# Performance work log

Hardware: AMD Instinct MI355X
Metric: run time of the kernel (lower is better)

The kernel has to match this reference:

```python
import jax, jax.numpy as jnp
import numpy as np

CD_COEFF = 1.0


def setup_inputs() -> dict:
    key = jax.random.key(0)
    k1, k2 = jax.random.split(key)
    x_diff_pred = jax.random.normal(k1, (16, 2048, 3), dtype=jnp.float32)
    x_diff_target = jax.random.normal(k2, (16, 2048, 3), dtype=jnp.float32)
    return {"x_diff_pred": x_diff_pred, "x_diff_target": x_diff_target}


def _chamfer(p1, p2):
    # p1: (bs, N, 3), p2: (bs, M, 3)
    # squared pairwise distances: (bs, N, M)
    diff = p1[:, :, None, :] - p2[:, None, :, :]
    d2 = jnp.sum(diff * diff, axis=-1)
    # bidirectional min reduction
    min_p1 = jnp.min(d2, axis=2)  # (bs, N): nearest target for each pred point
    min_p2 = jnp.min(d2, axis=1)  # (bs, M): nearest pred for each target point
    return jnp.mean(min_p1) + jnp.mean(min_p2)


def reference(x_diff_pred, x_diff_target):
    cd = _chamfer(x_diff_pred, x_diff_target)
    return CD_COEFF * cd
```

## Files before the change

kernel.cpp:

```cpp
#include <hip/hip_runtime.h>


#define NPTS  2048
#define BATCH 16
#define NBLK  256

__global__ __launch_bounds__(1024) void chamfer_kernel(
    const float* __restrict__ pred,
    const float* __restrict__ tgt,
    float* __restrict__ partial)
{
    const int bid = blockIdx.x;
    const int dir = bid >> 7;
    const int b   = (bid >> 3) & 15;
    const int qc  = bid & 7;

    const int tid  = threadIdx.x;
    const int lane = tid & 63;
    const int w    = tid >> 6;

    const float* __restrict__ P = dir ? tgt  : pred;
    const float* __restrict__ T = dir ? pred : tgt;
    const float* Pb = P + (size_t)b * NPTS * 3;
    const float* Tb = T + (size_t)b * NPTS * 3;

    __shared__ float4 tile[NPTS];
    __shared__ float  smin[16][256];
    __shared__ float  spart[4];

    #pragma unroll
    for (int k = 0; k < 2; ++k) {
        const int idx = tid + k * 1024;
        const float x = Tb[idx * 3 + 0];
        const float y = Tb[idx * 3 + 1];
        const float z = Tb[idx * 3 + 2];
        tile[idx] = make_float4(x, y, z, x * x + y * y + z * z);
    }

    float qx[4], qy[4], qz[4], pp[4], m0[4], m1[4];
    #pragma unroll
    for (int q = 0; q < 4; ++q) {
        const int qi = qc * 256 + q * 64 + lane;
        const float x = Pb[qi * 3 + 0];
        const float y = Pb[qi * 3 + 1];
        const float z = Pb[qi * 3 + 2];
        qx[q] = -2.0f * x;
        qy[q] = -2.0f * y;
        qz[q] = -2.0f * z;
        pp[q] = x * x + y * y + z * z;
        m0[q] = 3.4e38f;
        m1[q] = 3.4e38f;
    }

    __syncthreads();

    const int base = w * 128;
    #pragma unroll 2
    for (int j = 0; j < 128; j += 4) {
        const float4 ta = tile[base + j + 0];
        const float4 tb = tile[base + j + 1];
        const float4 tc = tile[base + j + 2];
        const float4 td = tile[base + j + 3];
        #pragma unroll
        for (int q = 0; q < 4; ++q) {
            const float da = fmaf(qz[q], ta.z, fmaf(qy[q], ta.y, fmaf(qx[q], ta.x, ta.w)));
            const float db = fmaf(qz[q], tb.z, fmaf(qy[q], tb.y, fmaf(qx[q], tb.x, tb.w)));
            const float dc = fmaf(qz[q], tc.z, fmaf(qy[q], tc.y, fmaf(qx[q], tc.x, tc.w)));
            const float dd = fmaf(qz[q], td.z, fmaf(qy[q], td.y, fmaf(qx[q], td.x, td.w)));
            m0[q] = fminf(fminf(m0[q], da), db);
            m1[q] = fminf(fminf(m1[q], dc), dd);
        }
    }

    #pragma unroll
    for (int q = 0; q < 4; ++q)
        smin[w][q * 64 + lane] = fminf(m0[q], m1[q]) + pp[q];
    __syncthreads();

    if (tid < 256) {
        float v = smin[0][tid];
        #pragma unroll
        for (int ww = 1; ww < 16; ++ww)
            v = fminf(v, smin[ww][tid]);
        #pragma unroll
        for (int off = 32; off > 0; off >>= 1)
            v += __shfl_down(v, off);
        if (lane == 0)
            spart[w] = v;
    }
    __syncthreads();

    if (tid == 0)
        partial[bid] = spart[0] + spart[1] + spart[2] + spart[3];
}

__global__ __launch_bounds__(256) void reduce_kernel(
    const float* __restrict__ partial,
    float* __restrict__ out)
{
    const int tid  = threadIdx.x;
    const int lane = tid & 63;
    const int w    = tid >> 6;
    __shared__ float s[4];

    float v = partial[tid];
    #pragma unroll
    for (int off = 32; off > 0; off >>= 1)
        v += __shfl_down(v, off);
    if (lane == 0) s[w] = v;
    __syncthreads();

    if (tid == 0)
        out[0] = (s[0] + s[1] + s[2] + s[3]) * (1.0f / (float)(BATCH * NPTS));
}

extern "C" void kernel_launch(void* const* d_in, const int* in_sizes, int n_in,
                              void* d_out, int out_size, void* d_ws, size_t ws_size,
                              hipStream_t stream)
{
    const float* pred = (const float*)d_in[0];
    const float* tgt  = (const float*)d_in[1];
    float* out = (float*)d_out;
    float* partial = (float*)d_ws;

    chamfer_kernel<<<dim3(NBLK), dim3(1024), 0, stream>>>(pred, tgt, partial);
    reduce_kernel<<<dim3(1), dim3(256), 0, stream>>>(partial, out);
}
```

Baseline: 17.72 us.

## Fuse final reduction into main kernel via last-block atomic counter; prefetch LDS tiles

Result: slower. 27.87 us (+57.3%).

```diff
diff --git a/kernel.cpp b/kernel.cpp
--- a/kernel.cpp
+++ b/kernel.cpp
@@ -8,7 +8,9 @@
 __global__ __launch_bounds__(1024) void chamfer_kernel(
     const float* __restrict__ pred,
     const float* __restrict__ tgt,
-    float* __restrict__ partial)
+    float* __restrict__ partial,
+    unsigned int* __restrict__ counter,
+    float* __restrict__ out)
 {
     const int bid = blockIdx.x;
     const int dir = bid >> 7;
@@ -27,6 +29,7 @@
     __shared__ float4 tile[NPTS];
     __shared__ float  smin[16][256];
     __shared__ float  spart[4];
+    __shared__ int    slast;
 
     #pragma unroll
     for (int k = 0; k < 2; ++k) {
@@ -55,12 +58,18 @@
     __syncthreads();
 
     const int base = w * 128;
+    float4 ta = tile[base + 0];
+    float4 tb = tile[base + 1];
+    float4 tc = tile[base + 2];
+    float4 td = tile[base + 3];
+
     #pragma unroll 2
     for (int j = 0; j < 128; j += 4) {
-        const float4 ta = tile[base + j + 0];
-        const float4 tb = tile[base + j + 1];
-        const float4 tc = tile[base + j + 2];
-        const float4 td = tile[base + j + 3];
+        const int nj = base + ((j + 4) & 127);
+        const float4 na = tile[nj + 0];
+        const float4 nb = tile[nj + 1];
+        const float4 nc = tile[nj + 2];
+        const float4 nd = tile[nj + 3];
         #pragma unroll
         for (int q = 0; q < 4; ++q) {
             const float da = fmaf(qz[q], ta.z, fmaf(qy[q], ta.y, fmaf(qx[q], ta.x, ta.w)));
@@ -70,6 +79,7 @@
             m0[q] = fminf(fminf(m0[q], da), db);
             m1[q] = fminf(fminf(m1[q], dc), dd);
         }
+        ta = na; tb = nb; tc = nc; td = nd;
     }
 
     #pragma unroll
@@ -90,28 +100,31 @@
     }
     __syncthreads();
 
-    if (tid == 0)
-        partial[bid] = spart[0] + spart[1] + spart[2] + spart[3];
-}
-
-__global__ __launch_bounds__(256) void reduce_kernel(
-    const float* __restrict__ partial,
-    float* __restrict__ out)
-{
-    const int tid  = threadIdx.x;
-    const int lane = tid & 63;
-    const int w    = tid >> 6;
-    __shared__ float s[4];
-
-    float v = partial[tid];
-    #pragma unroll
-    for (int off = 32; off > 0; off >>= 1)
-        v += __shfl_down(v, off);
-    if (lane == 0) s[w] = v;
+    if (tid == 0) {
+        const float s = spart[0] + spart[1] + spart[2] + spart[3];
+        __hip_atomic_store(&partial[bid], s, __ATOMIC_RELEASE,
+                           __HIP_MEMORY_SCOPE_AGENT);
+        const unsigned int old = __hip_atomic_fetch_add(
+            counter, 1u, __ATOMIC_ACQ_REL, __HIP_MEMORY_SCOPE_AGENT);
+        slast = (old == NBLK - 1);
+    }
     __syncthreads();
 
-    if (tid == 0)
-        out[0] = (s[0] + s[1] + s[2] + s[3]) * (1.0f / (float)(BATCH * NPTS));
+    if (slast) {
+        if (tid < 256) {
+            float v = __hip_atomic_load(&partial[tid], __ATOMIC_RELAXED,
+                                        __HIP_MEMORY_SCOPE_AGENT);
+            #pragma unroll
+            for (int off = 32; off > 0; off >>= 1)
+                v += __shfl_down(v, off);
+            if (lane == 0)
+                spart[w] = v;
+        }
+        __syncthreads();
+        if (tid == 0)
+            out[0] = (spart[0] + spart[1] + spart[2] + spart[3])
+                     * (1.0f / (float)(BATCH * NPTS));
+    }
 }
 
 extern "C" void kernel_launch(void* const* d_in, const int* in_sizes, int n_in,
@@ -122,7 +135,10 @@
     const float* tgt  = (const float*)d_in[1];
     float* out = (float*)d_out;
     float* partial = (float*)d_ws;
+    unsigned int* counter = (unsigned int*)((char*)d_ws + NBLK * sizeof(float));
 
-    chamfer_kernel<<<dim3(NBLK), dim3(1024), 0, stream>>>(pred, tgt, partial);
-    reduce_kernel<<<dim3(1), dim3(256), 0, stream>>>(partial, out);
+    hipMemsetAsync(counter, 0, sizeof(unsigned int), stream);
+
+    chamfer_kernel<<<dim3(NBLK), dim3(1024), 0, stream>>>(pred, tgt, partial,
+                                                          counter, out);
 }
```

## Split target set across block pairs and give each thread eight queries

Applied to the files above, without the earlier changes.

Result: slower. 22.58 us (+27.4%).

```diff
diff --git a/kernel.cpp b/kernel.cpp
--- a/kernel.cpp
+++ b/kernel.cpp
@@ -4,6 +4,8 @@
 #define NPTS  2048
 #define BATCH 16
 #define NBLK  256
+#define QPB   512
+#define TPB   1024
 
 __global__ __launch_bounds__(1024) void chamfer_kernel(
     const float* __restrict__ pred,
@@ -13,7 +15,8 @@
     const int bid = blockIdx.x;
     const int dir = bid >> 7;
     const int b   = (bid >> 3) & 15;
-    const int qc  = bid & 7;
+    const int qc  = (bid >> 1) & 3;
+    const int th  = bid & 1;
 
     const int tid  = threadIdx.x;
     const int lane = tid & 63;
@@ -22,25 +25,22 @@
     const float* __restrict__ P = dir ? tgt  : pred;
     const float* __restrict__ T = dir ? pred : tgt;
     const float* Pb = P + (size_t)b * NPTS * 3;
-    const float* Tb = T + (size_t)b * NPTS * 3;
+    const float* Tb = T + (size_t)b * NPTS * 3 + (size_t)th * TPB * 3;
 
-    __shared__ float4 tile[NPTS];
-    __shared__ float  smin[16][256];
-    __shared__ float  spart[4];
+    __shared__ float4 tile[TPB];
+    __shared__ float  smin[16][QPB];
 
-    #pragma unroll
-    for (int k = 0; k < 2; ++k) {
-        const int idx = tid + k * 1024;
-        const float x = Tb[idx * 3 + 0];
-        const float y = Tb[idx * 3 + 1];
-        const float z = Tb[idx * 3 + 2];
-        tile[idx] = make_float4(x, y, z, x * x + y * y + z * z);
+    {
+        const float x = Tb[tid * 3 + 0];
+        const float y = Tb[tid * 3 + 1];
+        const float z = Tb[tid * 3 + 2];
+        tile[tid] = make_float4(x, y, z, x * x + y * y + z * z);
     }
 
-    float qx[4], qy[4], qz[4], pp[4], m0[4], m1[4];
+    float qx[8], qy[8], qz[8], pp[8], m0[8], m1[8];
     #pragma unroll
-    for (int q = 0; q < 4; ++q) {
-        const int qi = qc * 256 + q * 64 + lane;
+    for (int q = 0; q < 8; ++q) {
+        const int qi = qc * QPB + q * 64 + lane;
         const float x = Pb[qi * 3 + 0];
         const float y = Pb[qi * 3 + 1];
         const float z = Pb[qi * 3 + 2];
@@ -54,15 +54,15 @@
 
     __syncthreads();
 
-    const int base = w * 128;
+    const int base = w * 64;
     #pragma unroll 2
-    for (int j = 0; j < 128; j += 4) {
+    for (int j = 0; j < 64; j += 4) {
         const float4 ta = tile[base + j + 0];
         const float4 tb = tile[base + j + 1];
         const float4 tc = tile[base + j + 2];
         const float4 td = tile[base + j + 3];
         #pragma unroll
-        for (int q = 0; q < 4; ++q) {
+        for (int q = 0; q < 8; ++q) {
             const float da = fmaf(qz[q], ta.z, fmaf(qy[q], ta.y, fmaf(qx[q], ta.x, ta.w)));
             const float db = fmaf(qz[q], tb.z, fmaf(qy[q], tb.y, fmaf(qx[q], tb.x, tb.w)));
             const float dc = fmaf(qz[q], tc.z, fmaf(qy[q], tc.y, fmaf(qx[q], tc.x, tc.w)));
@@ -73,45 +73,54 @@
     }
 
     #pragma unroll
-    for (int q = 0; q < 4; ++q)
+    for (int q = 0; q < 8; ++q)
         smin[w][q * 64 + lane] = fminf(m0[q], m1[q]) + pp[q];
     __syncthreads();
 
-    if (tid < 256) {
+    if (tid < QPB) {
         float v = smin[0][tid];
         #pragma unroll
         for (int ww = 1; ww < 16; ++ww)
             v = fminf(v, smin[ww][tid]);
-        #pragma unroll
-        for (int off = 32; off > 0; off >>= 1)
-            v += __shfl_down(v, off);
-        if (lane == 0)
-            spart[w] = v;
+        partial[bid * QPB + tid] = v;
     }
-    __syncthreads();
-
-    if (tid == 0)
-        partial[bid] = spart[0] + spart[1] + spart[2] + spart[3];
 }
 
-__global__ __launch_bounds__(256) void reduce_kernel(
+__global__ __launch_bounds__(1024) void reduce_kernel(
     const float* __restrict__ partial,
     float* __restrict__ out)
 {
     const int tid  = threadIdx.x;
     const int lane = tid & 63;
     const int w    = tid >> 6;
-    __shared__ float s[4];
+    __shared__ float s[16];
 
-    float v = partial[tid];
+    const float4* P4 = (const float4*)partial;
+    float acc = 0.0f;
+
+    #pragma unroll 4
+    for (int i = 0; i < 16; ++i) {
+        const int pairIdx = i * 1024 + tid;
+        const int g  = pairIdx >> 7;
+        const int q4 = pairIdx & 127;
+        const float4 va = P4[g * 256 + q4];
+        const float4 vb = P4[g * 256 + 128 + q4];
+        acc += fminf(va.x, vb.x) + fminf(va.y, vb.y)
+             + fminf(va.z, vb.z) + fminf(va.w, vb.w);
+    }
+
     #pragma unroll
     for (int off = 32; off > 0; off >>= 1)
-        v += __shfl_down(v, off);
-    if (lane == 0) s[w] = v;
+        acc += __shfl_down(acc, off);
+    if (lane == 0) s[w] = acc;
     __syncthreads();
 
-    if (tid == 0)
-        out[0] = (s[0] + s[1] + s[2] + s[3]) * (1.0f / (float)(BATCH * NPTS));
+    if (tid == 0) {
+        float t = 0.0f;
+        #pragma unroll
+        for (int ww = 0; ww < 16; ++ww) t += s[ww];
+        out[0] = t * (1.0f / (float)(BATCH * NPTS));
+    }
 }
 
 extern "C" void kernel_launch(void* const* d_in, const int* in_sizes, int n_in,
@@ -124,5 +133,5 @@
     float* partial = (float*)d_ws;
 
     chamfer_kernel<<<dim3(NBLK), dim3(1024), 0, stream>>>(pred, tgt, partial);
-    reduce_kernel<<<dim3(1), dim3(256), 0, stream>>>(partial, out);
+    reduce_kernel<<<dim3(1), dim3(1024), 0, stream>>>(partial, out);
 }
```
